# Kernel tuning notes

Hardware: AMD Instinct MI355X
Metric: run time of the kernel (lower is better)

Reference implementation:

```python
import jax, jax.numpy as jnp
import numpy as np

# Image grid matching params nImgX/nImgY; nImgZ == nDctY (slice-wise 2D parallel-beam BP)
NIMG_X = 512
NIMG_Y = 512


def _backproject(proj):
    """Pixel-driven 2D parallel-beam backprojection applied per slice.

    proj: (nView, Z, nDct) sinogram (views over [0, pi), unit detector/pixel spacing,
    detector and image both centered). Returns vol: (Z, NIMG_Y, NIMG_X),
    scaled by pi/nView (the weighting the original module applies, cf. its backward).
    """
    nView, Z, nDct = proj.shape
    thetas = jnp.arange(nView, dtype=jnp.float32) * (np.pi / nView)
    xs = jnp.arange(NIMG_X, dtype=jnp.float32) - (NIMG_X - 1) / 2.0
    ys = jnp.arange(NIMG_Y, dtype=jnp.float32) - (NIMG_Y - 1) / 2.0
    ctr = (nDct - 1) / 2.0

    def step(vol, inp):
        p, c, s = inp                      # p: (Z, nDct)
        t = xs[None, :] * c + ys[:, None] * s + ctr   # (Y, X) detector coordinate
        i0 = jnp.floor(t).astype(jnp.int32)
        w = t - i0.astype(jnp.float32)
        v0 = (i0 >= 0) & (i0 < nDct)
        v1 = ((i0 + 1) >= 0) & ((i0 + 1) < nDct)
        i0c = jnp.clip(i0, 0, nDct - 1)
        i1c = jnp.clip(i0 + 1, 0, nDct - 1)
        g0 = p[:, i0c]                      # (Z, Y, X) gather
        g1 = p[:, i1c]
        contrib = g0 * jnp.where(v0, 1.0 - w, 0.0)[None] + g1 * jnp.where(v1, w, 0.0)[None]
        return vol + contrib, None

    vol0 = jnp.zeros((Z, NIMG_Y, NIMG_X), dtype=proj.dtype)
    vol, _ = jax.lax.scan(step, vol0, (proj, jnp.cos(thetas), jnp.sin(thetas)))
    return vol * jnp.float32(np.pi / nView)


def setup_inputs() -> dict:
    key = jax.random.key(0)
    # sinogram: (nDctY=32 slices, 1, nView=720, nDctX=1024)
    x = jax.random.normal(key, (32, 1, 720, 1024), dtype=jnp.float32)
    return {"x": x}


def reference(x):
    # original: squeeze -> (Z, nView, nDct) -> transpose(1,0,2) -> (nView, Z, nDct)
    proj = jnp.transpose(x[:, 0], (1, 0, 2))
    vol = _backproject(proj)               # (Z, NIMG_Y, NIMG_X)
    return vol[:, None, :, :]              # (nImgZ, 1, nImgY, nImgX)
```

## Files before the change

kernel.cpp:

```cpp
#include <hip/hip_runtime.h>
#include <math.h>

#define NVIEW 720
#define NDCT  1024
#define NZ    32
#define NX    512
#define NY    512

#define TS   32
#define ZG   16
#define NR   48
#define RS   20
#define GSTRIDE ((size_t)NVIEW * NDCT * 16)

typedef unsigned int uint;

#if __has_builtin(__builtin_amdgcn_fdot2)
#define USE_FDOT2 1
typedef _Float16 half2v __attribute__((ext_vector_type(2)));
#else
#define USE_FDOT2 0
#endif

__device__ __forceinline__ uint f2bf_rne(float f) {
    uint u = __float_as_uint(f);
    return (u + 0x7fffu + ((u >> 16) & 1u)) >> 16;
}

__device__ __forceinline__ uint pack_word(float a, float b) {
#if USE_FDOT2
    union { _Float16 h[2]; uint u; } r;
    r.h[0] = (_Float16)a;
    r.h[1] = (_Float16)(b - a);
    return r.u;
#else
    uint lo = f2bf_rne(b - a);
    uint u  = (f2bf_rne(a) << 16) | lo;
    uint up = u + 0x10000u, um = u - 0x10000u;
    float e0 = fabsf(__uint_as_float(u)  - a);
    float e1 = fabsf(__uint_as_float(up) - a);
    float e2 = fabsf(__uint_as_float(um) - a);
    if (e1 < e0) { u = up; e0 = e1; }
    if (e2 < e0) { u = um; }
    return u;
#endif
}

__global__ __launch_bounds__(64) void pack_kernel(const float* __restrict__ x,
                                                  uint* __restrict__ packed) {
    __shared__ uint tr[64 * 33];
    const int l  = threadIdx.x;
    const int v  = blockIdx.x;
    const int ib = blockIdx.y * 64;
    const bool last = (ib + 64 >= NDCT);
    const float* rowbase = x + (size_t)v * NDCT + ib;

    float pre = 0.0f;
    if (l < NZ && !last) pre = rowbase[(size_t)l * (NVIEW * NDCT) + 64];

    for (int z = 0; z < NZ; ++z) {
        const float* r = rowbase + (size_t)z * (NVIEW * NDCT);
        float a   = r[l];
        float a64 = __shfl(pre, z);
        float b   = __shfl(a, l + 1);
        if (l == 63) b = a64;
        tr[l * 33 + z] = pack_word(a, b);
    }
    __syncthreads();

    #pragma unroll
    for (int it = 0; it < 8; ++it) {
        int c  = it * 64 + l;
        int il = c >> 3;
        int zc = (c & 7) * 4;
        int gg = zc >> 4;
        int zl = zc & 15;
        uint4 w4;
        w4.x = tr[il * 33 + zc + 0];
        w4.y = tr[il * 33 + zc + 1];
        w4.z = tr[il * 33 + zc + 2];
        w4.w = tr[il * 33 + zc + 3];
        uint* dst = packed + (size_t)gg * GSTRIDE
                  + ((size_t)(v * NDCT + ib + il) << 4) + zl;
        *(uint4*)dst = w4;
    }
}

#if USE_FDOT2
#define SAMP(A, zz, uu, WP, WF) do { \
    union { uint q; half2v h; } _c; _c.q = (uu); \
    A[zz] = __builtin_amdgcn_fdot2(_c.h, (WP), A[zz], false); \
} while (0)
#else
#define SAMP(A, zz, uu, WP, WF) do { \
    A[zz] += __uint_as_float(uu); \
    A[zz]  = fmaf((WF), __uint_as_float((uu) << 16), A[zz]); \
} while (0)
#endif

#define SAMPLE16(A, WP, WF) do { \
    SAMP(A, 0, q0.x, WP, WF); SAMP(A, 1, q0.y, WP, WF); \
    SAMP(A, 2, q0.z, WP, WF); SAMP(A, 3, q0.w, WP, WF); \
    SAMP(A, 4, q1.x, WP, WF); SAMP(A, 5, q1.y, WP, WF); \
    SAMP(A, 6, q1.z, WP, WF); SAMP(A, 7, q1.w, WP, WF); \
    SAMP(A, 8, q2.x, WP, WF); SAMP(A, 9, q2.y, WP, WF); \
    SAMP(A,10, q2.z, WP, WF); SAMP(A,11, q2.w, WP, WF); \
    SAMP(A,12, q3.x, WP, WF); SAMP(A,13, q3.y, WP, WF); \
    SAMP(A,14, q3.z, WP, WF); SAMP(A,15, q3.w, WP, WF); \
} while (0)

__global__ __launch_bounds__(512, 4) void bp_lds(const uint* __restrict__ packed,
                                                 float* __restrict__ out) {
    __shared__ float4 tab[NVIEW];
    __shared__ __align__(16) uint stage[2][NR * RS];

    const int tid = threadIdx.y * 16 + threadIdx.x;
    const int g   = blockIdx.z;
    const float xf0 = (float)(int)(blockIdx.x * TS) - 255.5f;
    const float yf0 = (float)(int)(blockIdx.y * TS) - 255.5f;

    for (int v = tid; v < NVIEW; v += 512) {
        float th = (float)v * (float)(M_PI / NVIEW);
        float s, c;
        sincosf(th, &s, &c);
        float b0 = fmaf(yf0, s, 511.5f);
        float b1 = fmaf(yf0 + (float)(TS - 1), s, 511.5f);
        float t00 = fmaf(xf0, c, b0);
        float t10 = fmaf(xf0 + (float)(TS - 1), c, b0);
        float t01 = fmaf(xf0, c, b1);
        float t11 = fmaf(xf0 + (float)(TS - 1), c, b1);
        int imin = (int)fminf(fminf(t00, t10), fminf(t01, t11));
        tab[v] = make_float4(c, s, 511.5f - (float)imin, __int_as_float(imin));
    }
    __syncthreads();

    const int x0 = blockIdx.x * TS + threadIdx.x * 2;
    const int y  = blockIdx.y * TS + threadIdx.y;
    const float xf = (float)x0 - 255.5f;
    const float yf = (float)y  - 255.5f;

    float acc0[ZG], acc1[ZG];
    #pragma unroll
    for (int z = 0; z < ZG; ++z) { acc0[z] = 0.0f; acc1[z] = 0.0f; }

    const int  wv   = tid >> 6;
    const int  ln   = tid & 63;
    const bool sact = (ln < 24);
    const int  slot = wv * 24 + ln;
    const int  sr   = slot >> 2;
    const int  sch  = slot & 3;
    const size_t sg_off = ((size_t)sr << 4) + (sch << 2);
    const int  swr  = sr * RS + (sch << 2);
    const uint* greg = packed + (size_t)g * GSTRIDE;

    float4 t4 = tab[0];
    uint4 st;
    if (sact) {
        st = *(const uint4*)(greg + ((size_t)__float_as_int(t4.w) << 4) + sg_off);
        *(uint4*)&stage[0][swr] = st;
    }
    __syncthreads();

    #pragma unroll 2
    for (int v = 0; v < NVIEW; ++v) {
        float4 t4n = t4;
        if (v + 1 < NVIEW) t4n = tab[v + 1];
        if (sact && v + 1 < NVIEW) {
            st = *(const uint4*)(greg + ((size_t)(v + 1) << 14)
                                 + ((size_t)__float_as_int(t4n.w) << 4) + sg_off);
        }

        const float c = t4.x;
        float t0 = fmaf(xf, c, fmaf(yf, t4.y, t4.z));
        float t1 = t0 + c;
        int   i0 = (int)t0;
        int   i1 = (int)t1;
        float w0 = t0 - (float)i0;
        float w1 = t1 - (float)i1;

#if USE_FDOT2
        half2v wp0; wp0[0] = (_Float16)1.0f; wp0[1] = (_Float16)w0;
        half2v wp1; wp1[0] = (_Float16)1.0f; wp1[1] = (_Float16)w1;
#else
        const int wp0 = 0, wp1 = 0;
#endif

        const uint* sp = stage[v & 1] + i0 * RS;
        uint4 q0 = *(const uint4*)(sp);
        uint4 q1 = *(const uint4*)(sp + 4);
        uint4 q2 = *(const uint4*)(sp + 8);
        uint4 q3 = *(const uint4*)(sp + 12);

        SAMPLE16(acc0, wp0, w0);

        if (i1 != i0) {
            const uint* sp1 = stage[v & 1] + i1 * RS;
            q0 = *(const uint4*)(sp1);
            q1 = *(const uint4*)(sp1 + 4);
            q2 = *(const uint4*)(sp1 + 8);
            q3 = *(const uint4*)(sp1 + 12);
        }

        SAMPLE16(acc1, wp1, w1);

        if (sact && v + 1 < NVIEW) *(uint4*)&stage[(v + 1) & 1][swr] = st;
        __syncthreads();
        t4 = t4n;
    }

    const float scale = 0.0043633231299858236f;
    #pragma unroll
    for (int lz = 0; lz < ZG; ++lz) {
        float2 o = make_float2(acc0[lz] * scale, acc1[lz] * scale);
        *(float2*)(out + (((size_t)(g * ZG + lz)) * NY + y) * NX + x0) = o;
    }
}

__global__ __launch_bounds__(256) void bp_direct(const float* __restrict__ xin,
                                                 float* __restrict__ out) {
    __shared__ float2 cs[NVIEW];
    int lt = threadIdx.y * 64 + threadIdx.x;
    for (int v = lt; v < NVIEW; v += 256) {
        float th = (float)v * (float)(M_PI / NVIEW);
        float s, c;
        sincosf(th, &s, &c);
        cs[v] = make_float2(c, s);
    }
    __syncthreads();

    int x = blockIdx.x * 64 + threadIdx.x;
    int y = blockIdx.y * 4 + threadIdx.y;
    float xf = (float)x - 255.5f;
    float yf = (float)y - 255.5f;

    float acc[NZ];
    #pragma unroll
    for (int z = 0; z < NZ; ++z) acc[z] = 0.0f;

    for (int v = 0; v < NVIEW; ++v) {
        float2 a = cs[v];
        float t  = fmaf(xf, a.x, fmaf(yf, a.y, 511.5f));
        int   i0 = (int)t;
        float w  = t - (float)i0;
        const float* p = xin + (size_t)v * NDCT + i0;
        #pragma unroll
        for (int z = 0; z < NZ; ++z) {
            float g0 = p[(size_t)z * NVIEW * NDCT];
            float g1 = p[(size_t)z * NVIEW * NDCT + 1];
            acc[z] += fmaf(w, g1 - g0, g0);
        }
    }

    const float scale = 0.0043633231299858236f;
    #pragma unroll
    for (int z = 0; z < NZ; ++z) {
        out[((size_t)z * NY + y) * NX + x] = acc[z] * scale;
    }
}

extern "C" void kernel_launch(void* const* d_in, const int* in_sizes, int n_in,
                              void* d_out, int out_size, void* d_ws, size_t ws_size,
                              hipStream_t stream) {
    const float* x = (const float*)d_in[0];
    float* out = (float*)d_out;

    const size_t packed_bytes = 2 * GSTRIDE * sizeof(uint);

    if (ws_size >= packed_bytes) {
        uint* packed = (uint*)d_ws;
        pack_kernel<<<dim3(NVIEW, NDCT / 64), 64, 0, stream>>>(x, packed);
        bp_lds<<<dim3(NX / TS, NY / TS, 2), dim3(16, 32), 0, stream>>>(packed, out);
    } else {
        bp_direct<<<dim3(NX / 64, NY / 4), dim3(64, 4), 0, stream>>>(x, out);
    }
}
```

Measured before the change: 717.7 us.

## Remap wavefronts to 16x8 pixel tiles and fetch second sample from global

Threads are remapped so each wavefront covers a 16x8 block of pixel pairs instead of 32x2 rows, which shrinks the detector footprint each wavefront touches. When the second pixel of a pair lands on a different detector bin, its packed data is now loaded directly from global memory and chosen with selects, instead of a second conditional LDS read. The intent is to cut LDS read traffic and divergence. The cost is extra global loads issued on every view, which depend on cache hits and add latency.

```diff
diff --git a/kernel.cpp b/kernel.cpp
--- a/kernel.cpp
+++ b/kernel.cpp
@@ -114,7 +114,7 @@
     __shared__ float4 tab[NVIEW];
     __shared__ __align__(16) uint stage[2][NR * RS];
 
-    const int tid = threadIdx.y * 16 + threadIdx.x;
+    const int tid = threadIdx.x;
     const int g   = blockIdx.z;
     const float xf0 = (float)(int)(blockIdx.x * TS) - 255.5f;
     const float yf0 = (float)(int)(blockIdx.y * TS) - 255.5f;
@@ -134,8 +134,12 @@
     }
     __syncthreads();
 
-    const int x0 = blockIdx.x * TS + threadIdx.x * 2;
-    const int y  = blockIdx.y * TS + threadIdx.y;
+    const int lane = tid & 63;
+    const int wv   = tid >> 6;
+    const int lx   = lane & 7, ly = lane >> 3;
+    const int xh   = wv & 1,   yq = wv >> 1;
+    const int x0   = blockIdx.x * TS + xh * 16 + lx * 2;
+    const int y    = blockIdx.y * TS + yq * 8 + ly;
     const float xf = (float)x0 - 255.5f;
     const float yf = (float)y  - 255.5f;
 
@@ -143,10 +147,8 @@
     #pragma unroll
     for (int z = 0; z < ZG; ++z) { acc0[z] = 0.0f; acc1[z] = 0.0f; }
 
-    const int  wv   = tid >> 6;
-    const int  ln   = tid & 63;
-    const bool sact = (ln < 24);
-    const int  slot = wv * 24 + ln;
+    const bool sact = (lane < 24);
+    const int  slot = wv * 24 + lane;
     const int  sr   = slot >> 2;
     const int  sch  = slot & 3;
     const size_t sg_off = ((size_t)sr << 4) + (sch << 2);
@@ -171,6 +173,7 @@
         }
 
         const float c = t4.x;
+        const int  imin_i = __float_as_int(t4.w);
         float t0 = fmaf(xf, c, fmaf(yf, t4.y, t4.z));
         float t1 = t0 + c;
         int   i0 = (int)t0;
@@ -185,6 +188,17 @@
         const int wp0 = 0, wp1 = 0;
 #endif
 
+        const bool m = (i1 != i0);
+        uint4 r0, r1, r2, r3;
+        if (m) {
+            const uint* gp = greg + ((size_t)v << 14)
+                           + ((size_t)(imin_i + i1) << 4);
+            r0 = *(const uint4*)(gp);
+            r1 = *(const uint4*)(gp + 4);
+            r2 = *(const uint4*)(gp + 8);
+            r3 = *(const uint4*)(gp + 12);
+        }
+
         const uint* sp = stage[v & 1] + i0 * RS;
         uint4 q0 = *(const uint4*)(sp);
         uint4 q1 = *(const uint4*)(sp + 4);
@@ -193,13 +207,14 @@
 
         SAMPLE16(acc0, wp0, w0);
 
-        if (i1 != i0) {
-            const uint* sp1 = stage[v & 1] + i1 * RS;
-            q0 = *(const uint4*)(sp1);
-            q1 = *(const uint4*)(sp1 + 4);
-            q2 = *(const uint4*)(sp1 + 8);
-            q3 = *(const uint4*)(sp1 + 12);
-        }
+        q0.x = m ? r0.x : q0.x; q0.y = m ? r0.y : q0.y;
+        q0.z = m ? r0.z : q0.z; q0.w = m ? r0.w : q0.w;
+        q1.x = m ? r1.x : q1.x; q1.y = m ? r1.y : q1.y;
+        q1.z = m ? r1.z : q1.z; q1.w = m ? r1.w : q1.w;
+        q2.x = m ? r2.x : q2.x; q2.y = m ? r2.y : q2.y;
+        q2.z = m ? r2.z : q2.z; q2.w = m ? r2.w : q2.w;
+        q3.x = m ? r3.x : q3.x; q3.y = m ? r3.y : q3.y;
+        q3.z = m ? r3.z : q3.z; q3.w = m ? r3.w : q3.w;
 
         SAMPLE16(acc1, wp1, w1);
 
@@ -269,7 +284,7 @@
     if (ws_size >= packed_bytes) {
         uint* packed = (uint*)d_ws;
         pack_kernel<<<dim3(NVIEW, NDCT / 64), 64, 0, stream>>>(x, packed);
-        bp_lds<<<dim3(NX / TS, NY / TS, 2), dim3(16, 32), 0, stream>>>(packed, out);
+        bp_lds<<<dim3(NX / TS, NY / TS, 2), dim3(512), 0, stream>>>(packed, out);
     } else {
         bp_direct<<<dim3(NX / 64, NY / 4), dim3(64, 4), 0, stream>>>(x, out);
     }
```

New measurement: 1.807 ms. +151.8%, slower.
